# Kernel tuning notes

Hardware: AMD Instinct MI355X
Metric: run time of the kernel (lower is better)

The kernel has to match this reference:

```python
import jax, jax.numpy as jnp
import numpy as np

N_NODES = 50000
N_EDGES = 800000
IN_CH, HID_CH, OUT_CH = 512, 256, 128


def setup_inputs() -> dict:
    key = jax.random.key(0)
    k = jax.random.split(key, 6)
    x = jax.random.normal(k[0], (N_NODES, IN_CH), dtype=jnp.float32)
    edge_index = jax.random.randint(k[1], (2, N_EDGES), 0, N_NODES, dtype=jnp.int64)
    # Glorot-ish scaled weights
    W0 = jax.random.normal(k[2], (IN_CH, HID_CH), dtype=jnp.float32) * (1.0 / np.sqrt(IN_CH))
    b0 = jnp.zeros((HID_CH,), dtype=jnp.float32)
    W1 = jax.random.normal(k[3], (HID_CH, OUT_CH), dtype=jnp.float32) * (1.0 / np.sqrt(HID_CH))
    b1 = jnp.zeros((OUT_CH,), dtype=jnp.float32)
    PW = jax.random.normal(k[4], (OUT_CH, OUT_CH), dtype=jnp.float32) * (1.0 / np.sqrt(OUT_CH))
    Pb = jnp.zeros((OUT_CH,), dtype=jnp.float32)
    return {"x": x, "edge_index": edge_index, "W0": W0, "b0": b0,
            "W1": W1, "b1": b1, "PW": PW, "Pb": Pb}


def reference(x, edge_index, W0, b0, W1, b1, PW, Pb):
    N = x.shape[0]
    # GCN normalization with added self-loops (edge_weight=None -> ones)
    loop = jnp.arange(N, dtype=edge_index.dtype)
    src = jnp.concatenate([edge_index[0], loop])  # [E+N]
    dst = jnp.concatenate([edge_index[1], loop])
    w = jnp.ones(src.shape[0], dtype=x.dtype)
    deg = jax.ops.segment_sum(w, dst, num_segments=N)  # in-degree incl. self-loop
    dinv = jnp.where(deg > 0, jax.lax.rsqrt(jnp.maximum(deg, 1e-12)), 0.0)
    norm = dinv[src] * dinv[dst]  # [E+N]

    def gcn_conv(h, W, b):
        hl = h @ W                               # [N, F_out] linear first (PyG GCNConv)
        msg = norm[:, None] * hl[src]            # gather + scale  [E+N, F_out]
        return jax.ops.segment_sum(msg, dst, num_segments=N) + b

    # eval mode: dropout is identity
    h = jax.nn.relu(gcn_conv(x, W0, b0))
    h = gcn_conv(h, W1, b1)                      # last layer: no relu
    p = h @ PW + Pb                              # PGE linear [N, OUT]
    vals = jnp.max(p, axis=0)                    # torch.max(dim=0) -> (values, indices)
    idx = jnp.argmax(p, axis=0)
    return (h, vals, idx)
```

## Files before the change

kernel.cpp:

```cpp
#include <hip/hip_runtime.h>
#include <stdint.h>

#define N_NODES 50000
#define N_EDGES 800000
#define IN_CH   512
#define HID_CH  256
#define OUT_CH  128
#define NPAD    50048
#define SLOT    96

#define NB_E   3125
#define NB2    391

#define PZ    25
#define PW0B  (PZ + 64)
#define PW1B  (PW0B + 16)
#define PPWB  (PW1B + 8)

typedef unsigned short ushort_t;
typedef __attribute__((ext_vector_type(8))) short    short8;
typedef __attribute__((ext_vector_type(4))) float    floatx4;
typedef __attribute__((ext_vector_type(4))) _Float16 half4v;
typedef __attribute__((ext_vector_type(2))) _Float16 half2v;

__device__ inline ushort_t f2bf(float x) {
    union { float f; unsigned u; } v; v.f = x;
    unsigned r = v.u + 0x7fffu + ((v.u >> 16) & 1u);
    return (ushort_t)(r >> 16);
}
__device__ inline float bf2f(ushort_t h) {
    union { unsigned u; float f; } v; v.u = ((unsigned)h) << 16;
    return v.f;
}
__device__ inline void gl_lds16(const void* g, void* l) {
    __builtin_amdgcn_global_load_lds((const __attribute__((address_space(1))) void*)g,
                                     (__attribute__((address_space(3))) void*)l, 16, 0, 0);
}

#define SWZ(r) ((((r) >> 1) & 3) << 3)

__device__ inline void conv_splitT8(const float* __restrict__ W,
                                    ushort_t* __restrict__ WhT,
                                    ushort_t* __restrict__ WlT,
                                    int K, int N, int base) {
    float4 v0 = *(const float4*)(W + base);
    float4 v1 = *(const float4*)(W + base + 4);
    float vv[8] = {v0.x, v0.y, v0.z, v0.w, v1.x, v1.y, v1.z, v1.w};
    #pragma unroll
    for (int j = 0; j < 8; ++j) {
        int g = base + j;
        int k = g / N, n = g - k * N;
        int ks = k ^ SWZ(n);
        ushort_t h = f2bf(vv[j]);
        WhT[(size_t)n * K + ks] = h;
        WlT[(size_t)n * K + ks] = f2bf(vv[j] - bf2f(h));
    }
}

__global__ __launch_bounds__(256) void k_prep(const float* __restrict__ W0,
                                              const float* __restrict__ W1,
                                              const float* __restrict__ PW,
                                              int* __restrict__ cnt,
                                              ushort_t* W0hT, ushort_t* W0lT,
                                              ushort_t* W1hT, ushort_t* W1lT,
                                              ushort_t* PWhT, ushort_t* PWlT) {
    int b = blockIdx.x, tid = threadIdx.x;
    if (b < PZ) {
        int base = b * 2048 + tid * 8;
        #pragma unroll
        for (int j = 0; j < 8; ++j)
            if (base + j < N_NODES) cnt[base + j] = 0;
    } else if (b < PW0B) {
        conv_splitT8(W0, W0hT, W0lT, IN_CH, HID_CH, (b - PZ) * 2048 + tid * 8);
    } else if (b < PW1B) {
        conv_splitT8(W1, W1hT, W1lT, HID_CH, OUT_CH, (b - PW0B) * 2048 + tid * 8);
    } else {
        conv_splitT8(PW, PWhT, PWlT, OUT_CH, OUT_CH, (b - PW1B) * 2048 + tid * 8);
    }
}

__global__ __launch_bounds__(256) void k_bucket(const int* __restrict__ esrc,
                                                const int* __restrict__ edst,
                                                int* __restrict__ cnt,
                                                int* __restrict__ slots) {
    int e = blockIdx.x * 256 + threadIdx.x;
    if (e < N_EDGES) {
        int d = edst[e];
        int c = atomicAdd(&cnt[d], 1);
        slots[(size_t)d * SLOT + c] = esrc[e];
    }
}

__global__ __launch_bounds__(256) void k_dinv(const int* __restrict__ cnt,
                                              float* __restrict__ dinv) {
    int i = blockIdx.x * 256 + threadIdx.x;
    if (i < N_NODES) dinv[i] = rsqrtf((float)cnt[i] + 1.0f);
}

__global__ __launch_bounds__(256) void gemm0_x(const float* __restrict__ A,
                                               const ushort_t* __restrict__ BhT,
                                               const ushort_t* __restrict__ BlT,
                                               _Float16* __restrict__ C,
                                               int M, int N, int K) {
    __shared__ ushort_t sm[4][128 * 32];
    const int tid  = threadIdx.x;
    const int wave = tid >> 6, lane = tid & 63;
    const int m0 = blockIdx.y * 128, n0 = blockIdx.x * 128;

    const int sr = tid >> 1, sseg = tid & 1;
    const float* gA = A + (size_t)min(m0 + sr, M - 1) * K + sseg * 16;
    const int swa = (sr >> 1) & 3;
    ushort_t* wh0 = &sm[0][sr * 32 + (((sseg * 2)     ^ swa) * 8)];
    ushort_t* wh1 = &sm[0][sr * 32 + (((sseg * 2 + 1) ^ swa) * 8)];
    ushort_t* wl0 = &sm[1][sr * 32 + (((sseg * 2)     ^ swa) * 8)];
    ushort_t* wl1 = &sm[1][sr * 32 + (((sseg * 2 + 1) ^ swa) * 8)];

    const int c0 = wave * 128 + lane, c1 = c0 + 64;
    const ushort_t* gbh0 = BhT + (size_t)(n0 + (c0 >> 2)) * K + (c0 & 3) * 8;
    const ushort_t* gbh1 = BhT + (size_t)(n0 + (c1 >> 2)) * K + (c1 & 3) * 8;
    const ushort_t* gbl0 = BlT + (size_t)(n0 + (c0 >> 2)) * K + (c0 & 3) * 8;
    const ushort_t* gbl1 = BlT + (size_t)(n0 + (c1 >> 2)) * K + (c1 & 3) * 8;
    ushort_t* lb0 = &sm[2][wave * 1024];  ushort_t* lb1 = &sm[2][wave * 1024 + 512];
    ushort_t* lc0 = &sm[3][wave * 1024];  ushort_t* lc1 = &sm[3][wave * 1024 + 512];

    floatx4 zero = {0.f, 0.f, 0.f, 0.f};
    floatx4 acc[4][4];
    #pragma unroll
    for (int i = 0; i < 4; ++i)
        #pragma unroll
        for (int j = 0; j < 4; ++j) acc[i][j] = zero;

    const int wm = (wave & 1) * 64, wn = (wave >> 1) * 64;
    const int fr = lane & 15, fq = lane >> 4;
    const int sx = SWZ(fr);

    for (int k0 = 0; k0 < K; k0 += 32) {
        gl_lds16(gbh0, lb0); gl_lds16(gbh1, lb1);
        gl_lds16(gbl0, lc0); gl_lds16(gbl1, lc1);
        gbh0 += 32; gbh1 += 32; gbl0 += 32; gbl1 += 32;
        float4 q0 = ((const float4*)gA)[0];
        float4 q1 = ((const float4*)gA)[1];
        float4 q2 = ((const float4*)gA)[2];
        float4 q3 = ((const float4*)gA)[3];
        gA += 32;
        float vv[16] = {q0.x, q0.y, q0.z, q0.w, q1.x, q1.y, q1.z, q1.w,
                        q2.x, q2.y, q2.z, q2.w, q3.x, q3.y, q3.z, q3.w};
        union { ushort_t u[8]; short8 v; } h0u, h1u, l0u, l1u;
        #pragma unroll
        for (int j = 0; j < 8; ++j) {
            ushort_t h = f2bf(vv[j]);
            h0u.u[j] = h; l0u.u[j] = f2bf(vv[j] - bf2f(h));
        }
        #pragma unroll
        for (int j = 0; j < 8; ++j) {
            ushort_t h = f2bf(vv[8 + j]);
            h1u.u[j] = h; l1u.u[j] = f2bf(vv[8 + j] - bf2f(h));
        }
        *(short8*)wh0 = h0u.v; *(short8*)wh1 = h1u.v;
        *(short8*)wl0 = l0u.v; *(short8*)wl1 = l1u.v;
        __syncthreads();
        short8 afh[4], afl[4], bfh[4], bfl[4];
        #pragma unroll
        for (int t = 0; t < 4; ++t) {
            int ai = (wm + t * 16 + fr) * 32 + (fq * 8 ^ sx);
            int bi = (wn + t * 16 + fr) * 32 + (fq * 8 ^ sx);
            afh[t] = *(const short8*)&sm[0][ai];
            afl[t] = *(const short8*)&sm[1][ai];
            bfh[t] = *(const short8*)&sm[2][bi];
            bfl[t] = *(const short8*)&sm[3][bi];
        }
        #pragma unroll
        for (int i = 0; i < 4; ++i)
            #pragma unroll
            for (int j = 0; j < 4; ++j) {
                acc[i][j] = __builtin_amdgcn_mfma_f32_16x16x32_bf16(afh[i], bfh[j], acc[i][j], 0, 0, 0);
                acc[i][j] = __builtin_amdgcn_mfma_f32_16x16x32_bf16(afh[i], bfl[j], acc[i][j], 0, 0, 0);
                acc[i][j] = __builtin_amdgcn_mfma_f32_16x16x32_bf16(afl[i], bfh[j], acc[i][j], 0, 0, 0);
            }
        __syncthreads();
    }
    const int colb = n0 + wn + fr;
    #pragma unroll
    for (int i = 0; i < 4; ++i) {
        int rowb = m0 + wm + i * 16 + fq * 4;
        #pragma unroll
        for (int r = 0; r < 4; ++r) {
            int row = rowb + r;
            if (row < M) {
                _Float16* cp = C + (size_t)row * N + colb;
                cp[0]  = (_Float16)acc[i][0][r];
                cp[16] = (_Float16)acc[i][1][r];
                cp[32] = (_Float16)acc[i][2][r];
                cp[48] = (_Float16)acc[i][3][r];
            }
        }
    }
}

__global__ __launch_bounds__(256) void gemm_bf(const ushort_t* __restrict__ Ah,
                                               const ushort_t* __restrict__ Al,
                                               const ushort_t* __restrict__ BhT,
                                               const ushort_t* __restrict__ BlT,
                                               _Float16* __restrict__ C,
                                               int M, int N, int K) {
    __shared__ ushort_t sm[4][128 * 32];
    const int tid  = threadIdx.x;
    const int wave = tid >> 6, lane = tid & 63;
    const int m0 = blockIdx.y * 128, n0 = blockIdx.x * 128;

    const int c0 = wave * 128 + lane, c1 = c0 + 64;
    const int ar0 = min(m0 + (c0 >> 2), M - 1), ar1 = min(m0 + (c1 >> 2), M - 1);
    const ushort_t* gah0 = Ah + (size_t)ar0 * K + (c0 & 3) * 8;
    const ushort_t* gah1 = Ah + (size_t)ar1 * K + (c1 & 3) * 8;
    const ushort_t* gal0 = Al + (size_t)ar0 * K + (c0 & 3) * 8;
    const ushort_t* gal1 = Al + (size_t)ar1 * K + (c1 & 3) * 8;
    const ushort_t* gbh0 = BhT + (size_t)(n0 + (c0 >> 2)) * K + (c0 & 3) * 8;
    const ushort_t* gbh1 = BhT + (size_t)(n0 + (c1 >> 2)) * K + (c1 & 3) * 8;
    const ushort_t* gbl0 = BlT + (size_t)(n0 + (c0 >> 2)) * K + (c0 & 3) * 8;
    const ushort_t* gbl1 = BlT + (size_t)(n0 + (c1 >> 2)) * K + (c1 & 3) * 8;
    ushort_t* la0 = &sm[0][wave * 1024];       ushort_t* la1 = &sm[0][wave * 1024 + 512];
    ushort_t* ll0 = &sm[1][wave * 1024];       ushort_t* ll1 = &sm[1][wave * 1024 + 512];
    ushort_t* lb0 = &sm[2][wave * 1024];       ushort_t* lb1 = &sm[2][wave * 1024 + 512];
    ushort_t* lc0 = &sm[3][wave * 1024];       ushort_t* lc1 = &sm[3][wave * 1024 + 512];

    floatx4 zero = {0.f, 0.f, 0.f, 0.f};
    floatx4 acc[4][4];
    #pragma unroll
    for (int i = 0; i < 4; ++i)
        #pragma unroll
        for (int j = 0; j < 4; ++j) acc[i][j] = zero;

    const int wm = (wave & 1) * 64, wn = (wave >> 1) * 64;
    const int fr = lane & 15, fq = lane >> 4;
    const int sx = SWZ(fr);

    for (int k0 = 0; k0 < K; k0 += 32) {
        gl_lds16(gah0, la0); gl_lds16(gah1, la1);
        gl_lds16(gal0, ll0); gl_lds16(gal1, ll1);
        gl_lds16(gbh0, lb0); gl_lds16(gbh1, lb1);
        gl_lds16(gbl0, lc0); gl_lds16(gbl1, lc1);
        gah0 += 32; gah1 += 32; gal0 += 32; gal1 += 32;
        gbh0 += 32; gbh1 += 32; gbl0 += 32; gbl1 += 32;
        __syncthreads();
        short8 afh[4], afl[4], bfh[4], bfl[4];
        #pragma unroll
        for (int t = 0; t < 4; ++t) {
            int ai = (wm + t * 16 + fr) * 32 + (fq * 8 ^ sx);
            int bi = (wn + t * 16 + fr) * 32 + (fq * 8 ^ sx);
            afh[t] = *(const short8*)&sm[0][ai];
            afl[t] = *(const short8*)&sm[1][ai];
            bfh[t] = *(const short8*)&sm[2][bi];
            bfl[t] = *(const short8*)&sm[3][bi];
        }
        #pragma unroll
        for (int i = 0; i < 4; ++i)
            #pragma unroll
            for (int j = 0; j < 4; ++j) {
                acc[i][j] = __builtin_amdgcn_mfma_f32_16x16x32_bf16(afh[i], bfh[j], acc[i][j], 0, 0, 0);
                acc[i][j] = __builtin_amdgcn_mfma_f32_16x16x32_bf16(afh[i], bfl[j], acc[i][j], 0, 0, 0);
                acc[i][j] = __builtin_amdgcn_mfma_f32_16x16x32_bf16(afl[i], bfh[j], acc[i][j], 0, 0, 0);
            }
        __syncthreads();
    }
    const int colb = n0 + wn + fr;
    #pragma unroll
    for (int i = 0; i < 4; ++i) {
        int rowb = m0 + wm + i * 16 + fq * 4;
        #pragma unroll
        for (int r = 0; r < 4; ++r) {
            int row = rowb + r;
            if (row < M) {
                _Float16* cp = C + (size_t)row * N + colb;
                cp[0]  = (_Float16)acc[i][0][r];
                cp[16] = (_Float16)acc[i][1][r];
                cp[32] = (_Float16)acc[i][2][r];
                cp[48] = (_Float16)acc[i][3][r];
            }
        }
    }
}

__global__ __launch_bounds__(256) void gemm_pge(const ushort_t* __restrict__ Ah,
                                                const ushort_t* __restrict__ Al,
                                                const ushort_t* __restrict__ BhT,
                                                const ushort_t* __restrict__ BlT,
                                                float* __restrict__ pv,
                                                int* __restrict__ pi,
                                                int M, int K) {
    __shared__ ushort_t sm[4][128 * 32];
    __shared__ float redv[8][128];
    __shared__ int   redi[8][128];
    const int tid  = threadIdx.x;
    const int wave = tid >> 6, lane = tid & 63;
    const int m0 = blockIdx.x * 128;

    const int c0 = wave * 128 + lane, c1 = c0 + 64;
    const int ar0 = min(m0 + (c0 >> 2), M - 1), ar1 = min(m0 + (c1 >> 2), M - 1);
    const ushort_t* gah0 = Ah + (size_t)ar0 * K + (c0 & 3) * 8;
    const ushort_t* gah1 = Ah + (size_t)ar1 * K + (c1 & 3) * 8;
    const ushort_t* gal0 = Al + (size_t)ar0 * K + (c0 & 3) * 8;
    const ushort_t* gal1 = Al + (size_t)ar1 * K + (c1 & 3) * 8;
    const ushort_t* gbh0 = BhT + (size_t)(c0 >> 2) * K + (c0 & 3) * 8;
    const ushort_t* gbh1 = BhT + (size_t)(c1 >> 2) * K + (c1 & 3) * 8;
    const ushort_t* gbl0 = BlT + (size_t)(c0 >> 2) * K + (c0 & 3) * 8;
    const ushort_t* gbl1 = BlT + (size_t)(c1 >> 2) * K + (c1 & 3) * 8;
    ushort_t* la0 = &sm[0][wave * 1024];       ushort_t* la1 = &sm[0][wave * 1024 + 512];
    ushort_t* ll0 = &sm[1][wave * 1024];       ushort_t* ll1 = &sm[1][wave * 1024 + 512];
    ushort_t* lb0 = &sm[2][wave * 1024];       ushort_t* lb1 = &sm[2][wave * 1024 + 512];
    ushort_t* lc0 = &sm[3][wave * 1024];       ushort_t* lc1 = &sm[3][wave * 1024 + 512];

    floatx4 zero = {0.f, 0.f, 0.f, 0.f};
    floatx4 acc[4][4];
    #pragma unroll
    for (int i = 0; i < 4; ++i)
        #pragma unroll
        for (int j = 0; j < 4; ++j) acc[i][j] = zero;

    const int wm = (wave & 1) * 64, wn = (wave >> 1) * 64;
    const int fr = lane & 15, fq = lane >> 4;
    const int sx = SWZ(fr);

    for (int k0 = 0; k0 < K; k0 += 32) {
        gl_lds16(gah0, la0); gl_lds16(gah1, la1);
        gl_lds16(gal0, ll0); gl_lds16(gal1, ll1);
        gl_lds16(gbh0, lb0); gl_lds16(gbh1, lb1);
        gl_lds16(gbl0, lc0); gl_lds16(gbl1, lc1);
        gah0 += 32; gah1 += 32; gal0 += 32; gal1 += 32;
        gbh0 += 32; gbh1 += 32; gbl0 += 32; gbl1 += 32;
        __syncthreads();
        short8 afh[4], afl[4], bfh[4], bfl[4];
        #pragma unroll
        for (int t = 0; t < 4; ++t) {
            int ai = (wm + t * 16 + fr) * 32 + (fq * 8 ^ sx);
            int bi = (wn + t * 16 + fr) * 32 + (fq * 8 ^ sx);
            afh[t] = *(const short8*)&sm[0][ai];
            afl[t] = *(const short8*)&sm[1][ai];
            bfh[t] = *(const short8*)&sm[2][bi];
            bfl[t] = *(const short8*)&sm[3][bi];
        }
        #pragma unroll
        for (int i = 0; i < 4; ++i)
            #pragma unroll
            for (int j = 0; j < 4; ++j) {
                acc[i][j] = __builtin_amdgcn_mfma_f32_16x16x32_bf16(afh[i], bfh[j], acc[i][j], 0, 0, 0);
                acc[i][j] = __builtin_amdgcn_mfma_f32_16x16x32_bf16(afh[i], bfl[j], acc[i][j], 0, 0, 0);
                acc[i][j] = __builtin_amdgcn_mfma_f32_16x16x32_bf16(afl[i], bfh[j], acc[i][j], 0, 0, 0);
            }
        __syncthreads();
    }
    const int slot = (wave & 1) * 4 + fq;
    #pragma unroll
    for (int j = 0; j < 4; ++j) {
        float bv = -3.402823466e+38f; int bidx = 0;
        #pragma unroll
        for (int i = 0; i < 4; ++i) {
            int rowb = m0 + wm + i * 16 + fq * 4;
            #pragma unroll
            for (int r = 0; r < 4; ++r) {
                int row = rowb + r;
                float v = acc[i][j][r];
                if (row < M && v > bv) { bv = v; bidx = row; }
            }
        }
        redv[slot][wn + j * 16 + fr] = bv;
        redi[slot][wn + j * 16 + fr] = bidx;
    }
    __syncthreads();
    if (tid < 128) {
        float bv = redv[0][tid]; int bidx = redi[0][tid];
        #pragma unroll
        for (int s = 1; s < 8; ++s) {
            float v = redv[s][tid]; int ix = redi[s][tid];
            if (v > bv || (v == bv && ix < bidx)) { bv = v; bidx = ix; }
        }
        pv[blockIdx.x * 128 + tid] = bv;
        pi[blockIdx.x * 128 + tid] = bidx;
    }
}

__global__ __launch_bounds__(256) void agg256_relu_bf(const _Float16* __restrict__ hl,
                                                      const float* __restrict__ dinv,
                                                      const int* __restrict__ cnt,
                                                      const int* __restrict__ slots,
                                                      const float* __restrict__ bias,
                                                      ushort_t* __restrict__ oh,
                                                      ushort_t* __restrict__ ol) {
    int d = blockIdx.x * 4 + (threadIdx.x >> 6);
    int lane = threadIdx.x & 63;
    float di = dinv[d];
    half4v v = ((const half4v*)(hl + (size_t)d * 256))[lane];
    float w = di * di;
    float ax = w * (float)v[0], ay = w * (float)v[1];
    float az = w * (float)v[2], aw = w * (float)v[3];
    const int* sl = slots + (size_t)d * SLOT;
    int n = cnt[d];
    int e = 0;
    for (; e + 8 <= n; e += 8) {
        int s[8]; half4v u[8]; float ws[8];
        #pragma unroll
        for (int j = 0; j < 8; ++j) s[j] = sl[e + j];
        #pragma unroll
        for (int j = 0; j < 8; ++j) u[j] = ((const half4v*)(hl + (size_t)s[j] * 256))[lane];
        #pragma unroll
        for (int j = 0; j < 8; ++j) ws[j] = dinv[s[j]] * di;
        #pragma unroll
        for (int j = 0; j < 8; ++j) {
            ax += ws[j] * (float)u[j][0]; ay += ws[j] * (float)u[j][1];
            az += ws[j] * (float)u[j][2]; aw += ws[j] * (float)u[j][3];
        }
    }
    for (; e < n; ++e) {
        int s = sl[e];
        float ws = dinv[s] * di;
        half4v u = ((const half4v*)(hl + (size_t)s * 256))[lane];
        ax += ws * (float)u[0]; ay += ws * (float)u[1];
        az += ws * (float)u[2]; aw += ws * (float)u[3];
    }
    float4 b = ((const float4*)bias)[lane];
    float rx = fmaxf(ax + b.x, 0.0f), ry = fmaxf(ay + b.y, 0.0f);
    float rz = fmaxf(az + b.z, 0.0f), rw = fmaxf(aw + b.w, 0.0f);
    ushort4 hv, lv;
    hv.x = f2bf(rx); lv.x = f2bf(rx - bf2f(hv.x));
    hv.y = f2bf(ry); lv.y = f2bf(ry - bf2f(hv.y));
    hv.z = f2bf(rz); lv.z = f2bf(rz - bf2f(hv.z));
    hv.w = f2bf(rw); lv.w = f2bf(rw - bf2f(hv.w));
    int sidx = (lane * 4) ^ SWZ(d);
    *(ushort4*)&oh[(size_t)d * 256 + sidx] = hv;
    *(ushort4*)&ol[(size_t)d * 256 + sidx] = lv;
}

__global__ __launch_bounds__(256) void agg128_bias_bf(const _Float16* __restrict__ hl,
                                                      const float* __restrict__ dinv,
                                                      const int* __restrict__ cnt,
                                                      const int* __restrict__ slots,
                                                      const float* __restrict__ bias,
                                                      float* __restrict__ out,
                                                      ushort_t* __restrict__ oh,
                                                      ushort_t* __restrict__ ol) {
    int d = blockIdx.x * 4 + (threadIdx.x >> 6);
    int lane = threadIdx.x & 63;
    float di = dinv[d];
    half2v v = ((const half2v*)(hl + (size_t)d * 128))[lane];
    float w = di * di;
    float ax = w * (float)v[0], ay = w * (float)v[1];
    const int* sl = slots + (size_t)d * SLOT;
    int n = cnt[d];
    int e = 0;
    for (; e + 8 <= n; e += 8) {
        int s[8]; half2v u[8]; float ws[8];
        #pragma unroll
        for (int j = 0; j < 8; ++j) s[j] = sl[e + j];
        #pragma unroll
        for (int j = 0; j < 8; ++j) u[j] = ((const half2v*)(hl + (size_t)s[j] * 128))[lane];
        #pragma unroll
        for (int j = 0; j < 8; ++j) ws[j] = dinv[s[j]] * di;
        #pragma unroll
        for (int j = 0; j < 8; ++j) { ax += ws[j] * (float)u[j][0]; ay += ws[j] * (float)u[j][1]; }
    }
    for (; e < n; ++e) {
        int s = sl[e];
        float ws = dinv[s] * di;
        half2v u = ((const half2v*)(hl + (size_t)s * 128))[lane];
        ax += ws * (float)u[0]; ay += ws * (float)u[1];
    }
    float2 b = ((const float2*)bias)[lane];
    float rx = ax + b.x, ry = ay + b.y;
    ((float2*)(out + (size_t)d * 128))[lane] = make_float2(rx, ry);
    ushort2 hv, lv;
    hv.x = f2bf(rx); lv.x = f2bf(rx - bf2f(hv.x));
    hv.y = f2bf(ry); lv.y = f2bf(ry - bf2f(hv.y));
    int sidx = (lane * 2) ^ SWZ(d);
    *(ushort2*)&oh[(size_t)d * 128 + sidx] = hv;
    *(ushort2*)&ol[(size_t)d * 128 + sidx] = lv;
}

__global__ __launch_bounds__(256) void k_reduce2(const float* __restrict__ pv,
                                                 const int* __restrict__ pi,
                                                 const float* __restrict__ Pb,
                                                 float* __restrict__ out) {
    int c = threadIdx.x & 127, sub = threadIdx.x >> 7;
    float best = -3.402823466e+38f;
    int bi = 0;
    for (int b = sub; b < NB2; b += 2) {
        float v = pv[b * 128 + c];
        int ix = pi[b * 128 + c];
        if (v > best || (v == best && ix < bi)) { best = v; bi = ix; }
    }
    __shared__ float sv[128];
    __shared__ int   si[128];
    if (sub == 1) { sv[c] = best; si[c] = bi; }
    __syncthreads();
    if (sub == 0) {
        float v1 = sv[c]; int i1 = si[c];
        if (v1 > best || (v1 == best && i1 < bi)) { best = v1; bi = i1; }
        out[(size_t)N_NODES * OUT_CH + c]       = best + Pb[c];
        out[(size_t)N_NODES * OUT_CH + 128 + c] = (float)bi;
    }
}

extern "C" void kernel_launch(void* const* d_in, const int* in_sizes, int n_in,
                              void* d_out, int out_size, void* d_ws, size_t ws_size,
                              hipStream_t stream) {
    const float* x  = (const float*)d_in[0];
    const int*   ei = (const int*)d_in[1];
    const float* W0 = (const float*)d_in[2];
    const float* b0 = (const float*)d_in[3];
    const float* W1 = (const float*)d_in[4];
    const float* b1 = (const float*)d_in[5];
    const float* PW = (const float*)d_in[6];
    const float* Pb = (const float*)d_in[7];
    float* out = (float*)d_out;
    const int* esrc = ei;
    const int* edst = ei + N_EDGES;

    char* w = (char*)d_ws;
    size_t off = 0;
    auto alloc = [&](size_t bytes) -> void* {
        void* p = (void*)(w + off);
        off = (off + bytes + 255) & ~(size_t)255;
        return p;
    };
    int*       cnt    = (int*)alloc((size_t)N_NODES * 4);
    float*     dinv   = (float*)alloc((size_t)N_NODES * 4);
    int*       slots  = (int*)alloc((size_t)N_NODES * SLOT * 4);
    float*     pmax_v = (float*)alloc((size_t)NB2 * 128 * 4);
    int*       pmax_i = (int*)alloc((size_t)NB2 * 128 * 4);
    _Float16*  bufH   = (_Float16*)alloc((size_t)NPAD * 256 * 2);
    ushort_t*  h0h    = (ushort_t*)alloc((size_t)N_NODES * HID_CH * 2);
    ushort_t*  h0l    = (ushort_t*)alloc((size_t)N_NODES * HID_CH * 2);
    ushort_t*  h1h    = (ushort_t*)alloc((size_t)N_NODES * OUT_CH * 2);
    ushort_t*  h1l    = (ushort_t*)alloc((size_t)N_NODES * OUT_CH * 2);
    ushort_t*  W0hT   = (ushort_t*)alloc((size_t)IN_CH * HID_CH * 2);
    ushort_t*  W0lT   = (ushort_t*)alloc((size_t)IN_CH * HID_CH * 2);
    ushort_t*  W1hT   = (ushort_t*)alloc((size_t)HID_CH * OUT_CH * 2);
    ushort_t*  W1lT   = (ushort_t*)alloc((size_t)HID_CH * OUT_CH * 2);
    ushort_t*  PWhT   = (ushort_t*)alloc((size_t)OUT_CH * OUT_CH * 2);
    ushort_t*  PWlT   = (ushort_t*)alloc((size_t)OUT_CH * OUT_CH * 2);

    k_prep<<<PPWB, 256, 0, stream>>>(W0, W1, PW, cnt,
                                     W0hT, W0lT, W1hT, W1lT, PWhT, PWlT);
    k_bucket<<<NB_E, 256, 0, stream>>>(esrc, edst, cnt, slots);
    k_dinv<<<196, 256, 0, stream>>>(cnt, dinv);

    gemm0_x<<<dim3(HID_CH / 128, NB2), 256, 0, stream>>>(
        x, W0hT, W0lT, bufH, N_NODES, HID_CH, IN_CH);
    agg256_relu_bf<<<N_NODES / 4, 256, 0, stream>>>(bufH, dinv, cnt, slots, b0, h0h, h0l);

    gemm_bf<<<dim3(1, NB2), 256, 0, stream>>>(
        h0h, h0l, W1hT, W1lT, bufH, N_NODES, OUT_CH, HID_CH);
    agg128_bias_bf<<<N_NODES / 4, 256, 0, stream>>>(bufH, dinv, cnt, slots, b1,
                                                    out, h1h, h1l);

    gemm_pge<<<NB2, 256, 0, stream>>>(h1h, h1l, PWhT, PWlT, pmax_v, pmax_i,
                                      N_NODES, OUT_CH);
    k_reduce2<<<1, 256, 0, stream>>>(pmax_v, pmax_i, Pb, out);

    (void)in_sizes; (void)n_in; (void)out_size; (void)ws_size;
}
```

Before: 460.2 us.

## Double-buffer GEMM LDS tiles and fold source dinv scaling into GEMM epilogue

All three split-bf16 GEMMs now use two LDS buffers, issuing the next K-tile's global-to-LDS loads before computing the current one, with explicit waitcnt/barrier macros and launch bounds requesting two blocks per CU. The GEMM epilogues pre-scale each output row by dinv, so the aggregation kernels no longer gather dinv per neighbour and instead apply the destination dinv once at the end. The aggregation loops become a single masked 8-wide loop in place of a main loop plus scalar tail. The cost is double the LDS footprint and hand-written waitcnt counts that must be exact to stay correct.

Result: faster. 446.6 us (-2.9%).

```diff
diff --git a/kernel.cpp b/kernel.cpp
--- a/kernel.cpp
+++ b/kernel.cpp
@@ -38,6 +38,12 @@
 }
 
 #define SWZ(r) ((((r) >> 1) & 3) << 3)
+
+#define SYNC_PIPE(N) do {                                                    \
+    asm volatile("s_waitcnt vmcnt(" #N ") lgkmcnt(0)" ::: "memory");         \
+    __builtin_amdgcn_sched_barrier(0);                                       \
+    __builtin_amdgcn_s_barrier();                                            \
+    __builtin_amdgcn_sched_barrier(0); } while (0)
 
 __device__ inline void conv_splitT8(const float* __restrict__ W,
                                     ushort_t* __restrict__ WhT,
@@ -97,31 +103,60 @@
     if (i < N_NODES) dinv[i] = rsqrtf((float)cnt[i] + 1.0f);
 }
 
-__global__ __launch_bounds__(256) void gemm0_x(const float* __restrict__ A,
-                                               const ushort_t* __restrict__ BhT,
-                                               const ushort_t* __restrict__ BlT,
-                                               _Float16* __restrict__ C,
-                                               int M, int N, int K) {
-    __shared__ ushort_t sm[4][128 * 32];
+__global__ __launch_bounds__(256, 2) void gemm0_x(const float* __restrict__ A,
+                                                  const ushort_t* __restrict__ BhT,
+                                                  const ushort_t* __restrict__ BlT,
+                                                  const float* __restrict__ dinv,
+                                                  _Float16* __restrict__ C,
+                                                  int M, int N) {
+    constexpr int KT = IN_CH;
+    constexpr int NT = KT / 32;
+    __shared__ ushort_t sm[2][4][128 * 32];
     const int tid  = threadIdx.x;
     const int wave = tid >> 6, lane = tid & 63;
     const int m0 = blockIdx.y * 128, n0 = blockIdx.x * 128;
 
     const int sr = tid >> 1, sseg = tid & 1;
-    const float* gA = A + (size_t)min(m0 + sr, M - 1) * K + sseg * 16;
+    const float* gA = A + (size_t)min(m0 + sr, M - 1) * KT + sseg * 16;
     const int swa = (sr >> 1) & 3;
-    ushort_t* wh0 = &sm[0][sr * 32 + (((sseg * 2)     ^ swa) * 8)];
-    ushort_t* wh1 = &sm[0][sr * 32 + (((sseg * 2 + 1) ^ swa) * 8)];
-    ushort_t* wl0 = &sm[1][sr * 32 + (((sseg * 2)     ^ swa) * 8)];
-    ushort_t* wl1 = &sm[1][sr * 32 + (((sseg * 2 + 1) ^ swa) * 8)];
+    const int wo0 = sr * 32 + (((sseg * 2)     ^ swa) * 8);
+    const int wo1 = sr * 32 + (((sseg * 2 + 1) ^ swa) * 8);
 
     const int c0 = wave * 128 + lane, c1 = c0 + 64;
-    const ushort_t* gbh0 = BhT + (size_t)(n0 + (c0 >> 2)) * K + (c0 & 3) * 8;
-    const ushort_t* gbh1 = BhT + (size_t)(n0 + (c1 >> 2)) * K + (c1 & 3) * 8;
-    const ushort_t* gbl0 = BlT + (size_t)(n0 + (c0 >> 2)) * K + (c0 & 3) * 8;
-    const ushort_t* gbl1 = BlT + (size_t)(n0 + (c1 >> 2)) * K + (c1 & 3) * 8;
-    ushort_t* lb0 = &sm[2][wave * 1024];  ushort_t* lb1 = &sm[2][wave * 1024 + 512];
-    ushort_t* lc0 = &sm[3][wave * 1024];  ushort_t* lc1 = &sm[3][wave * 1024 + 512];
+    const ushort_t* gbh0 = BhT + (size_t)(n0 + (c0 >> 2)) * KT + (c0 & 3) * 8;
+    const ushort_t* gbh1 = BhT + (size_t)(n0 + (c1 >> 2)) * KT + (c1 & 3) * 8;
+    const ushort_t* gbl0 = BlT + (size_t)(n0 + (c0 >> 2)) * KT + (c0 & 3) * 8;
+    const ushort_t* gbl1 = BlT + (size_t)(n0 + (c1 >> 2)) * KT + (c1 & 3) * 8;
+    const int lo0 = wave * 1024, lo1 = wave * 1024 + 512;
+
+    float4 q0, q1, q2, q3;
+    auto loadA = [&]() {
+        q0 = ((const float4*)gA)[0]; q1 = ((const float4*)gA)[1];
+        q2 = ((const float4*)gA)[2]; q3 = ((const float4*)gA)[3];
+        gA += 32;
+    };
+    auto stageB = [&](int buf) {
+        gl_lds16(gbh0, &sm[buf][2][lo0]); gl_lds16(gbh1, &sm[buf][2][lo1]);
+        gl_lds16(gbl0, &sm[buf][3][lo0]); gl_lds16(gbl1, &sm[buf][3][lo1]);
+        gbh0 += 32; gbh1 += 32; gbl0 += 32; gbl1 += 32;
+    };
+    auto writeA = [&](int buf) {
+        float vv[16] = {q0.x, q0.y, q0.z, q0.w, q1.x, q1.y, q1.z, q1.w,
+                        q2.x, q2.y, q2.z, q2.w, q3.x, q3.y, q3.z, q3.w};
+        union { ushort_t u[8]; short8 v; } h0u, h1u, l0u, l1u;
+        #pragma unroll
+        for (int j = 0; j < 8; ++j) {
+            ushort_t h = f2bf(vv[j]);
+            h0u.u[j] = h; l0u.u[j] = f2bf(vv[j] - bf2f(h));
+        }
+        #pragma unroll
+        for (int j = 0; j < 8; ++j) {
+            ushort_t h = f2bf(vv[8 + j]);
+            h1u.u[j] = h; l1u.u[j] = f2bf(vv[8 + j] - bf2f(h));
+        }
+        *(short8*)&sm[buf][0][wo0] = h0u.v; *(short8*)&sm[buf][0][wo1] = h1u.v;
+        *(short8*)&sm[buf][1][wo0] = l0u.v; *(short8*)&sm[buf][1][wo1] = l1u.v;
+    };
 
     floatx4 zero = {0.f, 0.f, 0.f, 0.f};
     floatx4 acc[4][4];
@@ -134,40 +169,33 @@
     const int fr = lane & 15, fq = lane >> 4;
     const int sx = SWZ(fr);
 
-    for (int k0 = 0; k0 < K; k0 += 32) {
-        gl_lds16(gbh0, lb0); gl_lds16(gbh1, lb1);
-        gl_lds16(gbl0, lc0); gl_lds16(gbl1, lc1);
-        gbh0 += 32; gbh1 += 32; gbl0 += 32; gbl1 += 32;
-        float4 q0 = ((const float4*)gA)[0];
-        float4 q1 = ((const float4*)gA)[1];
-        float4 q2 = ((const float4*)gA)[2];
-        float4 q3 = ((const float4*)gA)[3];
-        gA += 32;
-        float vv[16] = {q0.x, q0.y, q0.z, q0.w, q1.x, q1.y, q1.z, q1.w,
-                        q2.x, q2.y, q2.z, q2.w, q3.x, q3.y, q3.z, q3.w};
-        union { ushort_t u[8]; short8 v; } h0u, h1u, l0u, l1u;
-        #pragma unroll
-        for (int j = 0; j < 8; ++j) {
-            ushort_t h = f2bf(vv[j]);
-            h0u.u[j] = h; l0u.u[j] = f2bf(vv[j] - bf2f(h));
-        }
-        #pragma unroll
-        for (int j = 0; j < 8; ++j) {
-            ushort_t h = f2bf(vv[8 + j]);
-            h1u.u[j] = h; l1u.u[j] = f2bf(vv[8 + j] - bf2f(h));
-        }
-        *(short8*)wh0 = h0u.v; *(short8*)wh1 = h1u.v;
-        *(short8*)wl0 = l0u.v; *(short8*)wl1 = l1u.v;
-        __syncthreads();
+    loadA();
+    stageB(0);
+    writeA(0);
+    loadA();
+    asm volatile("s_waitcnt vmcnt(4) lgkmcnt(0)" ::: "memory");
+    __builtin_amdgcn_sched_barrier(0);
+    __builtin_amdgcn_s_barrier();
+    __builtin_amdgcn_sched_barrier(0);
+
+    #pragma unroll 2
+    for (int t = 0; t < NT; ++t) {
+        const int cur = t & 1, nxt = cur ^ 1;
+        if (t + 1 < NT) stageB(nxt);
         short8 afh[4], afl[4], bfh[4], bfl[4];
         #pragma unroll
-        for (int t = 0; t < 4; ++t) {
-            int ai = (wm + t * 16 + fr) * 32 + (fq * 8 ^ sx);
-            int bi = (wn + t * 16 + fr) * 32 + (fq * 8 ^ sx);
-            afh[t] = *(const short8*)&sm[0][ai];
-            afl[t] = *(const short8*)&sm[1][ai];
-            bfh[t] = *(const short8*)&sm[2][bi];
-            bfl[t] = *(const short8*)&sm[3][bi];
+        for (int tt = 0; tt < 4; ++tt) {
+            int ai = (wm + tt * 16 + fr) * 32 + (fq * 8 ^ sx);
+            int bi = (wn + tt * 16 + fr) * 32 + (fq * 8 ^ sx);
+            afh[tt] = *(const short8*)&sm[cur][0][ai];
+            afl[tt] = *(const short8*)&sm[cur][1][ai];
+            bfh[tt] = *(const short8*)&sm[cur][2][bi];
+            bfl[tt] = *(const short8*)&sm[cur][3][bi];
+        }
+        if (t + 1 < NT) {
+            writeA(nxt);
+            __builtin_amdgcn_sched_barrier(0);
+            if (t + 2 < NT) loadA();
         }
         #pragma unroll
         for (int i = 0; i < 4; ++i)
@@ -177,7 +205,10 @@
                 acc[i][j] = __builtin_amdgcn_mfma_f32_16x16x32_bf16(afh[i], bfl[j], acc[i][j], 0, 0, 0);
                 acc[i][j] = __builtin_amdgcn_mfma_f32_16x16x32_bf16(afl[i], bfh[j], acc[i][j], 0, 0, 0);
             }
-        __syncthreads();
+        if (t + 1 < NT) {
+            if (t + 2 < NT) SYNC_PIPE(4);
+            else            SYNC_PIPE(0);
+        }
     }
     const int colb = n0 + wn + fr;
     #pragma unroll
@@ -187,41 +218,51 @@
         for (int r = 0; r < 4; ++r) {
             int row = rowb + r;
             if (row < M) {
+                float dv = dinv[row];
                 _Float16* cp = C + (size_t)row * N + colb;
-                cp[0]  = (_Float16)acc[i][0][r];
-                cp[16] = (_Float16)acc[i][1][r];
-                cp[32] = (_Float16)acc[i][2][r];
-                cp[48] = (_Float16)acc[i][3][r];
+                cp[0]  = (_Float16)(acc[i][0][r] * dv);
+                cp[16] = (_Float16)(acc[i][1][r] * dv);
+                cp[32] = (_Float16)(acc[i][2][r] * dv);
+                cp[48] = (_Float16)(acc[i][3][r] * dv);
             }
         }
     }
 }
 
-__global__ __launch_bounds__(256) void gemm_bf(const ushort_t* __restrict__ Ah,
-                                               const ushort_t* __restrict__ Al,
-                                               const ushort_t* __restrict__ BhT,
-                                               const ushort_t* __restrict__ BlT,
-                                               _Float16* __restrict__ C,
-                                               int M, int N, int K) {
-    __shared__ ushort_t sm[4][128 * 32];
+template <int KT>
+__global__ __launch_bounds__(256, 2) void gemm_bf(const ushort_t* __restrict__ Ah,
+                                                  const ushort_t* __restrict__ Al,
+                                                  const ushort_t* __restrict__ BhT,
+                                                  const ushort_t* __restrict__ BlT,
+                                                  const float* __restrict__ dinv,
+                                                  _Float16* __restrict__ C,
+                                                  int M, int N) {
+    constexpr int NT = KT / 32;
+    __shared__ ushort_t sm[2][4][128 * 32];
     const int tid  = threadIdx.x;
     const int wave = tid >> 6, lane = tid & 63;
     const int m0 = blockIdx.y * 128, n0 = blockIdx.x * 128;
 
     const int c0 = wave * 128 + lane, c1 = c0 + 64;
     const int ar0 = min(m0 + (c0 >> 2), M - 1), ar1 = min(m0 + (c1 >> 2), M - 1);
-    const ushort_t* gah0 = Ah + (size_t)ar0 * K + (c0 & 3) * 8;
-    const ushort_t* gah1 = Ah + (size_t)ar1 * K + (c1 & 3) * 8;
-    const ushort_t* gal0 = Al + (size_t)ar0 * K + (c0 & 3) * 8;
-    const ushort_t* gal1 = Al + (size_t)ar1 * K + (c1 & 3) * 8;
-    const ushort_t* gbh0 = BhT + (size_t)(n0 + (c0 >> 2)) * K + (c0 & 3) * 8;
-    const ushort_t* gbh1 = BhT + (size_t)(n0 + (c1 >> 2)) * K + (c1 & 3) * 8;
-    const ushort_t* gbl0 = BlT + (size_t)(n0 + (c0 >> 2)) * K + (c0 & 3) * 8;
-    const ushort_t* gbl1 = BlT + (size_t)(n0 + (c1 >> 2)) * K + (c1 & 3) * 8;
-    ushort_t* la0 = &sm[0][wave * 1024];       ushort_t* la1 = &sm[0][wave * 1024 + 512];
-    ushort_t* ll0 = &sm[1][wave * 1024];       ushort_t* ll1 = &sm[1][wave * 1024 + 512];
-    ushort_t* lb0 = &sm[2][wave * 1024];       ushort_t* lb1 = &sm[2][wave * 1024 + 512];
-    ushort_t* lc0 = &sm[3][wave * 1024];       ushort_t* lc1 = &sm[3][wave * 1024 + 512];
+    const ushort_t* gah0 = Ah + (size_t)ar0 * KT + (c0 & 3) * 8;
+    const ushort_t* gah1 = Ah + (size_t)ar1 * KT + (c1 & 3) * 8;
+    const ushort_t* gal0 = Al + (size_t)ar0 * KT + (c0 & 3) * 8;
+    const ushort_t* gal1 = Al + (size_t)ar1 * KT + (c1 & 3) * 8;
+    const ushort_t* gbh0 = BhT + (size_t)(n0 + (c0 >> 2)) * KT + (c0 & 3) * 8;
+    const ushort_t* gbh1 = BhT + (size_t)(n0 + (c1 >> 2)) * KT + (c1 & 3) * 8;
+    const ushort_t* gbl0 = BlT + (size_t)(n0 + (c0 >> 2)) * KT + (c0 & 3) * 8;
+    const ushort_t* gbl1 = BlT + (size_t)(n0 + (c1 >> 2)) * KT + (c1 & 3) * 8;
+    const int lo0 = wave * 1024, lo1 = wave * 1024 + 512;
+
+    auto stage = [&](int buf) {
+        gl_lds16(gah0, &sm[buf][0][lo0]); gl_lds16(gah1, &sm[buf][0][lo1]);
+        gl_lds16(gal0, &sm[buf][1][lo0]); gl_lds16(gal1, &sm[buf][1][lo1]);
+        gl_lds16(gbh0, &sm[buf][2][lo0]); gl_lds16(gbh1, &sm[buf][2][lo1]);
+        gl_lds16(gbl0, &sm[buf][3][lo0]); gl_lds16(gbl1, &sm[buf][3][lo1]);
+        gah0 += 32; gah1 += 32; gal0 += 32; gal1 += 32;
+        gbh0 += 32; gbh1 += 32; gbl0 += 32; gbl1 += 32;
+    };
 
     floatx4 zero = {0.f, 0.f, 0.f, 0.f};
     floatx4 acc[4][4];
@@ -234,23 +275,22 @@
     const int fr = lane & 15, fq = lane >> 4;
     const int sx = SWZ(fr);
 
-    for (int k0 = 0; k0 < K; k0 += 32) {
-        gl_lds16(gah0, la0); gl_lds16(gah1, la1);
-        gl_lds16(gal0, ll0); gl_lds16(gal1, ll1);
-        gl_lds16(gbh0, lb0); gl_lds16(gbh1, lb1);
-        gl_lds16(gbl0, lc0); gl_lds16(gbl1, lc1);
-        gah0 += 32; gah1 += 32; gal0 += 32; gal1 += 32;
-        gbh0 += 32; gbh1 += 32; gbl0 += 32; gbl1 += 32;
-        __syncthreads();
+    stage(0);
+    SYNC_PIPE(0);
+
+    #pragma unroll 2
+    for (int t = 0; t < NT; ++t) {
+        const int cur = t & 1, nxt = cur ^ 1;
+        if (t + 1 < NT) stage(nxt);
         short8 afh[4], afl[4], bfh[4], bfl[4];
         #pragma unroll
-        for (int t = 0; t < 4; ++t) {
-            int ai = (wm + t * 16 + fr) * 32 + (fq * 8 ^ sx);
-            int bi = (wn + t * 16 + fr) * 32 + (fq * 8 ^ sx);
-            afh[t] = *(const short8*)&sm[0][ai];
-            afl[t] = *(const short8*)&sm[1][ai];
-            bfh[t] = *(const short8*)&sm[2][bi];
-            bfl[t] = *(const short8*)&sm[3][bi];
+        for (int tt = 0; tt < 4; ++tt) {
+            int ai = (wm + tt * 16 + fr) * 32 + (fq * 8 ^ sx);
+            int bi = (wn + tt * 16 + fr) * 32 + (fq * 8 ^ sx);
+            afh[tt] = *(const short8*)&sm[cur][0][ai];
+            afl[tt] = *(const short8*)&sm[cur][1][ai];
+            bfh[tt] = *(const short8*)&sm[cur][2][bi];
+            bfl[tt] = *(const short8*)&sm[cur][3][bi];
         }
         #pragma unroll
         for (int i = 0; i < 4; ++i)
@@ -260,7 +300,7 @@
                 acc[i][j] = __builtin_amdgcn_mfma_f32_16x16x32_bf16(afh[i], bfl[j], acc[i][j], 0, 0, 0);
                 acc[i][j] = __builtin_amdgcn_mfma_f32_16x16x32_bf16(afl[i], bfh[j], acc[i][j], 0, 0, 0);
             }
-        __syncthreads();
+        if (t + 1 < NT) SYNC_PIPE(0);
     }
     const int colb = n0 + wn + fr;
     #pragma unroll
@@ -270,24 +310,27 @@
         for (int r = 0; r < 4; ++r) {
             int row = rowb + r;
             if (row < M) {
+                float dv = dinv[row];
                 _Float16* cp = C + (size_t)row * N + colb;
-                cp[0]  = (_Float16)acc[i][0][r];
-                cp[16] = (_Float16)acc[i][1][r];
-                cp[32] = (_Float16)acc[i][2][r];
-                cp[48] = (_Float16)acc[i][3][r];
+                cp[0]  = (_Float16)(acc[i][0][r] * dv);
+                cp[16] = (_Float16)(acc[i][1][r] * dv);
+                cp[32] = (_Float16)(acc[i][2][r] * dv);
+                cp[48] = (_Float16)(acc[i][3][r] * dv);
             }
         }
     }
 }
 
-__global__ __launch_bounds__(256) void gemm_pge(const ushort_t* __restrict__ Ah,
-                                                const ushort_t* __restrict__ Al,
-                                                const ushort_t* __restrict__ BhT,
-                                                const ushort_t* __restrict__ BlT,
-                                                float* __restrict__ pv,
-                                                int* __restrict__ pi,
-                                                int M, int K) {
-    __shared__ ushort_t sm[4][128 * 32];
+__global__ __launch_bounds__(256, 2) void gemm_pge(const ushort_t* __restrict__ Ah,
+                                                   const ushort_t* __restrict__ Al,
+                                                   const ushort_t* __restrict__ BhT,
+                                                   const ushort_t* __restrict__ BlT,
+                                                   float* __restrict__ pv,
+                                                   int* __restrict__ pi,
+                                                   int M) {
+    constexpr int KT = OUT_CH;
+    constexpr int NT = KT / 32;
+    __shared__ ushort_t sm[2][4][128 * 32];
     __shared__ float redv[8][128];
     __shared__ int   redi[8][128];
     const int tid  = threadIdx.x;
@@ -296,18 +339,24 @@
 
     const int c0 = wave * 128 + lane, c1 = c0 + 64;
     const int ar0 = min(m0 + (c0 >> 2), M - 1), ar1 = min(m0 + (c1 >> 2), M - 1);
-    const ushort_t* gah0 = Ah + (size_t)ar0 * K + (c0 & 3) * 8;
-    const ushort_t* gah1 = Ah + (size_t)ar1 * K + (c1 & 3) * 8;
-    const ushort_t* gal0 = Al + (size_t)ar0 * K + (c0 & 3) * 8;
-    const ushort_t* gal1 = Al + (size_t)ar1 * K + (c1 & 3) * 8;
-    const ushort_t* gbh0 = BhT + (size_t)(c0 >> 2) * K + (c0 & 3) * 8;
-    const ushort_t* gbh1 = BhT + (size_t)(c1 >> 2) * K + (c1 & 3) * 8;
-    const ushort_t* gbl0 = BlT + (size_t)(c0 >> 2) * K + (c0 & 3) * 8;
-    const ushort_t* gbl1 = BlT + (size_t)(c1 >> 2) * K + (c1 & 3) * 8;
-    ushort_t* la0 = &sm[0][wave * 1024];       ushort_t* la1 = &sm[0][wave * 1024 + 512];
-    ushort_t* ll0 = &sm[1][wave * 1024];       ushort_t* ll1 = &sm[1][wave * 1024 + 512];
-    ushort_t* lb0 = &sm[2][wave * 1024];       ushort_t* lb1 = &sm[2][wave * 1024 + 512];
-    ushort_t* lc0 = &sm[3][wave * 1024];       ushort_t* lc1 = &sm[3][wave * 1024 + 512];
+    const ushort_t* gah0 = Ah + (size_t)ar0 * KT + (c0 & 3) * 8;
+    const ushort_t* gah1 = Ah + (size_t)ar1 * KT + (c1 & 3) * 8;
+    const ushort_t* gal0 = Al + (size_t)ar0 * KT + (c0 & 3) * 8;
+    const ushort_t* gal1 = Al + (size_t)ar1 * KT + (c1 & 3) * 8;
+    const ushort_t* gbh0 = BhT + (size_t)(c0 >> 2) * KT + (c0 & 3) * 8;
+    const ushort_t* gbh1 = BhT + (size_t)(c1 >> 2) * KT + (c1 & 3) * 8;
+    const ushort_t* gbl0 = BlT + (size_t)(c0 >> 2) * KT + (c0 & 3) * 8;
+    const ushort_t* gbl1 = BlT + (size_t)(c1 >> 2) * KT + (c1 & 3) * 8;
+    const int lo0 = wave * 1024, lo1 = wave * 1024 + 512;
+
+    auto stage = [&](int buf) {
+        gl_lds16(gah0, &sm[buf][0][lo0]); gl_lds16(gah1, &sm[buf][0][lo1]);
+        gl_lds16(gal0, &sm[buf][1][lo0]); gl_lds16(gal1, &sm[buf][1][lo1]);
+        gl_lds16(gbh0, &sm[buf][2][lo0]); gl_lds16(gbh1, &sm[buf][2][lo1]);
+        gl_lds16(gbl0, &sm[buf][3][lo0]); gl_lds16(gbl1, &sm[buf][3][lo1]);
+        gah0 += 32; gah1 += 32; gal0 += 32; gal1 += 32;
+        gbh0 += 32; gbh1 += 32; gbl0 += 32; gbl1 += 32;
+    };
 
     floatx4 zero = {0.f, 0.f, 0.f, 0.f};
     floatx4 acc[4][4];
@@ -320,23 +369,22 @@
     const int fr = lane & 15, fq = lane >> 4;
     const int sx = SWZ(fr);
 
-    for (int k0 = 0; k0 < K; k0 += 32) {
-        gl_lds16(gah0, la0); gl_lds16(gah1, la1);
-        gl_lds16(gal0, ll0); gl_lds16(gal1, ll1);
-        gl_lds16(gbh0, lb0); gl_lds16(gbh1, lb1);
-        gl_lds16(gbl0, lc0); gl_lds16(gbl1, lc1);
-        gah0 += 32; gah1 += 32; gal0 += 32; gal1 += 32;
-        gbh0 += 32; gbh1 += 32; gbl0 += 32; gbl1 += 32;
-        __syncthreads();
+    stage(0);
+    SYNC_PIPE(0);
+
+    #pragma unroll 2
+    for (int t = 0; t < NT; ++t) {
+        const int cur = t & 1, nxt = cur ^ 1;
+        if (t + 1 < NT) stage(nxt);
         short8 afh[4], afl[4], bfh[4], bfl[4];
         #pragma unroll
-        for (int t = 0; t < 4; ++t) {
-            int ai = (wm + t * 16 + fr) * 32 + (fq * 8 ^ sx);
-            int bi = (wn + t * 16 + fr) * 32 + (fq * 8 ^ sx);
-            afh[t] = *(const short8*)&sm[0][ai];
-            afl[t] = *(const short8*)&sm[1][ai];
-            bfh[t] = *(const short8*)&sm[2][bi];
-            bfl[t] = *(const short8*)&sm[3][bi];
+        for (int tt = 0; tt < 4; ++tt) {
+            int ai = (wm + tt * 16 + fr) * 32 + (fq * 8 ^ sx);
+            int bi = (wn + tt * 16 + fr) * 32 + (fq * 8 ^ sx);
+            afh[tt] = *(const short8*)&sm[cur][0][ai];
+            afl[tt] = *(const short8*)&sm[cur][1][ai];
+            bfh[tt] = *(const short8*)&sm[cur][2][bi];
+            bfl[tt] = *(const short8*)&sm[cur][3][bi];
         }
         #pragma unroll
         for (int i = 0; i < 4; ++i)
@@ -346,8 +394,9 @@
                 acc[i][j] = __builtin_amdgcn_mfma_f32_16x16x32_bf16(afh[i], bfl[j], acc[i][j], 0, 0, 0);
                 acc[i][j] = __builtin_amdgcn_mfma_f32_16x16x32_bf16(afl[i], bfh[j], acc[i][j], 0, 0, 0);
             }
-        __syncthreads();
-    }
+        if (t + 1 < NT) SYNC_PIPE(0);
+    }
+    __syncthreads();
     const int slot = (wave & 1) * 4 + fq;
     #pragma unroll
     for (int j = 0; j < 4; ++j) {
@@ -389,36 +438,28 @@
     int lane = threadIdx.x & 63;
     float di = dinv[d];
     half4v v = ((const half4v*)(hl + (size_t)d * 256))[lane];
-    float w = di * di;
-    float ax = w * (float)v[0], ay = w * (float)v[1];
-    float az = w * (float)v[2], aw = w * (float)v[3];
+    float ax = (float)v[0], ay = (float)v[1], az = (float)v[2], aw = (float)v[3];
     const int* sl = slots + (size_t)d * SLOT;
     int n = cnt[d];
-    int e = 0;
-    for (; e + 8 <= n; e += 8) {
-        int s[8]; half4v u[8]; float ws[8];
-        #pragma unroll
-        for (int j = 0; j < 8; ++j) s[j] = sl[e + j];
+    for (int e = 0; e < n; e += 8) {
+        int s[8]; float m[8]; half4v u[8];
+        #pragma unroll
+        for (int j = 0; j < 8; ++j) {
+            bool live = (e + j) < n;
+            s[j] = live ? sl[e + j] : d;
+            m[j] = live ? 1.0f : 0.0f;
+        }
         #pragma unroll
         for (int j = 0; j < 8; ++j) u[j] = ((const half4v*)(hl + (size_t)s[j] * 256))[lane];
         #pragma unroll
-        for (int j = 0; j < 8; ++j) ws[j] = dinv[s[j]] * di;
-        #pragma unroll
         for (int j = 0; j < 8; ++j) {
-            ax += ws[j] * (float)u[j][0]; ay += ws[j] * (float)u[j][1];
-            az += ws[j] * (float)u[j][2]; aw += ws[j] * (float)u[j][3];
-        }
-    }
-    for (; e < n; ++e) {
-        int s = sl[e];
-        float ws = dinv[s] * di;
-        half4v u = ((const half4v*)(hl + (size_t)s * 256))[lane];
-        ax += ws * (float)u[0]; ay += ws * (float)u[1];
-        az += ws * (float)u[2]; aw += ws * (float)u[3];
+            ax += m[j] * (float)u[j][0]; ay += m[j] * (float)u[j][1];
+            az += m[j] * (float)u[j][2]; aw += m[j] * (float)u[j][3];
+        }
     }
     float4 b = ((const float4*)bias)[lane];
-    float rx = fmaxf(ax + b.x, 0.0f), ry = fmaxf(ay + b.y, 0.0f);
-    float rz = fmaxf(az + b.z, 0.0f), rw = fmaxf(aw + b.w, 0.0f);
+    float rx = fmaxf(fmaf(di, ax, b.x), 0.0f), ry = fmaxf(fmaf(di, ay, b.y), 0.0f);
+    float rz = fmaxf(fmaf(di, az, b.z), 0.0f), rw = fmaxf(fmaf(di, aw, b.w), 0.0f);
     ushort4 hv, lv;
     hv.x = f2bf(rx); lv.x = f2bf(rx - bf2f(hv.x));
     hv.y = f2bf(ry); lv.y = f2bf(ry - bf2f(hv.y));
@@ -441,30 +482,24 @@
     int lane = threadIdx.x & 63;
     float di = dinv[d];
     half2v v = ((const half2v*)(hl + (size_t)d * 128))[lane];
-    float w = di * di;
-    float ax = w * (float)v[0], ay = w * (float)v[1];
+    float ax = (float)v[0], ay = (float)v[1];
     const int* sl = slots + (size_t)d * SLOT;
     int n = cnt[d];
-    int e = 0;
-    for (; e + 8 <= n; e += 8) {
-        int s[8]; half2v u[8]; float ws[8];
-        #pragma unroll
-        for (int j = 0; j < 8; ++j) s[j] = sl[e + j];
+    for (int e = 0; e < n; e += 8) {
+        int s[8]; float m[8]; half2v u[8];
+        #pragma unroll
+        for (int j = 0; j < 8; ++j) {
+            bool live = (e + j) < n;
+            s[j] = live ? sl[e + j] : d;
+            m[j] = live ? 1.0f : 0.0f;
+        }
         #pragma unroll
         for (int j = 0; j < 8; ++j) u[j] = ((const half2v*)(hl + (size_t)s[j] * 128))[lane];
         #pragma unroll
-        for (int j = 0; j < 8; ++j) ws[j] = dinv[s[j]] * di;
-        #pragma unroll
-        for (int j = 0; j < 8; ++j) { ax += ws[j] * (float)u[j][0]; ay += ws[j] * (float)u[j][1]; }
-    }
-    for (; e < n; ++e) {
-        int s = sl[e];
-        float ws = dinv[s] * di;
-        half2v u = ((const half2v*)(hl + (size_t)s * 128))[lane];
-        ax += ws * (float)u[0]; ay += ws * (float)u[1];
+        for (int j = 0; j < 8; ++j) { ax += m[j] * (float)u[j][0]; ay += m[j] * (float)u[j][1]; }
     }
     float2 b = ((const float2*)bias)[lane];
-    float rx = ax + b.x, ry = ay + b.y;
+    float rx = fmaf(di, ax, b.x), ry = fmaf(di, ay, b.y);
     ((float2*)(out + (size_t)d * 128))[lane] = make_float2(rx, ry);
     ushort2 hv, lv;
     hv.x = f2bf(rx); lv.x = f2bf(rx - bf2f(hv.x));
@@ -543,16 +578,15 @@
     k_dinv<<<196, 256, 0, stream>>>(cnt, dinv);
 
     gemm0_x<<<dim3(HID_CH / 128, NB2), 256, 0, stream>>>(
-        x, W0hT, W0lT, bufH, N_NODES, HID_CH, IN_CH);
+        x, W0hT, W0lT, dinv, bufH, N_NODES, HID_CH);
     agg256_relu_bf<<<N_NODES / 4, 256, 0, stream>>>(bufH, dinv, cnt, slots, b0, h0h, h0l);
 
-    gemm_bf<<<dim3(1, NB2), 256, 0, stream>>>(
-        h0h, h0l, W1hT, W1lT, bufH, N_NODES, OUT_CH, HID_CH);
+    gemm_bf<HID_CH><<<dim3(1, NB2), 256, 0, stream>>>(
+        h0h, h0l, W1hT, W1lT, dinv, bufH, N_NODES, OUT_CH);
     agg128_bias_bf<<<N_NODES / 4, 256, 0, stream>>>(bufH, dinv, cnt, slots, b1,
                                                     out, h1h, h1l);
 
-    gemm_pge<<<NB2, 256, 0, stream>>>(h1h, h1l, PWhT, PWlT, pmax_v, pmax_i,
-                                      N_NODES, OUT_CH);
+    gemm_pge<<<NB2, 256, 0, stream>>>(h1h, h1l, PWhT, PWlT, pmax_v, pmax_i, N_NODES);
     k_reduce2<<<1, 256, 0, stream>>>(pmax_v, pmax_i, Pb, out);
 
     (void)in_sizes; (void)n_in; (void)out_size; (void)ws_size;
```
